# Kernel optimization log

Measured on AMD Instinct MI355X. Metric: run time of the kernel, lower is better.

The kernel has to match this reference:

```python
import jax, jax.numpy as jnp
import numpy as np


def _diffuse(x, A):
    # x: [B,C,N,L], A: [B,V,W] -> out[b,c,v,l] = sum_w x[b,c,w,l] * A[b,v,w]
    return jnp.einsum('ncwl,nvw->ncvl', x, A)


def setup_inputs() -> dict:
    key = jax.random.key(0)
    kx, k0, k1, k2, kw = jax.random.split(key, 5)
    B, C, N, L = 32, 40, 512, 12
    C_OUT = 20
    C_CAT = 7 * C  # (order*support_len + 1) * c_in = (2*3+1)*40
    x = jax.random.normal(kx, (B, C, N, L), dtype=jnp.float32)
    def mk_support(k):
        a = jax.random.uniform(k, (B, N, N), dtype=jnp.float32)
        return a / jnp.sum(a, axis=-1, keepdims=True)  # row-normalized transition
    A0, A1, A2 = mk_support(k0), mk_support(k1), mk_support(k2)
    # Conv2d(c_cat, c_out, kernel=(1,2), dilation=2) weights, stored [c_out, c_cat, 2]
    W = jax.random.normal(kw, (C_OUT, C_CAT, 2), dtype=jnp.float32) * 0.05
    b = jnp.zeros((C_OUT,), dtype=jnp.float32)
    return {'x': x, 'A0': A0, 'A1': A1, 'A2': A2, 'W': W, 'b': b}


def reference(x, A0, A1, A2, W, b):
    # dgcn.forward (eval mode, dropout is identity): order=2, support_len=3
    out = [x]
    for A in (A0, A1, A2):
        x1 = _diffuse(x, A)
        out.append(x1)
        x2 = _diffuse(x1, A)
        out.append(x2)
    h = jnp.concatenate(out, axis=1)  # [B, 7C, N, L]
    # linear_: Conv2d kernel (1,2), dilation 2, no padding -> taps at t and t+2, L_out = L-2
    y = (jnp.einsum('ncvl,oc->novl', h[..., :-2], W[:, :, 0])
         + jnp.einsum('ncvl,oc->novl', h[..., 2:], W[:, :, 1])
         + b[None, :, None, None])
    return y
```

## Files before the change

kernel.cpp:

```cpp
#include <hip/hip_runtime.h>
#include <hip/hip_bf16.h>


typedef unsigned short u16;
typedef u16 u16x4 __attribute__((ext_vector_type(4)));
typedef u16 u16x8 __attribute__((ext_vector_type(8)));
typedef __bf16 bf16x8 __attribute__((ext_vector_type(8)));
typedef float f32x4 __attribute__((ext_vector_type(4)));

__device__ __forceinline__ u16 f2bf(float f) {
    unsigned int u = __float_as_uint(f);
    u += 0x7fffu + ((u >> 16) & 1u);
    return (u16)(u >> 16);
}
__device__ __forceinline__ float bf2f(u16 h) {
    return __uint_as_float(((unsigned int)h) << 16);
}

__global__ __launch_bounds__(256) void proj_x(
    const float* __restrict__ x, const float* __restrict__ W,
    u16* __restrict__ P1, u16* __restrict__ P2, float* __restrict__ proj0)
{
    __shared__ u16 sA[144 * 104];
    __shared__ u16 sB[64 * 104];
    const int t = threadIdx.x;
    const int v0 = blockIdx.x * 64, l = blockIdx.y, b = blockIdx.z;

    for (int id = t; id < 144 * 13; id += 256) {
        int m = id / 13, kc = id % 13, k0 = kc * 8;
        u16x8 val = {};
        if (m < 140 && k0 < 80) {
            int o = m % 20, sg = m / 20;
            const float* wp = W + o * 560 + sg * 80 + k0;
            float4 w0 = *(const float4*)wp;
            float4 w1 = *(const float4*)(wp + 4);
            val[0] = f2bf(w0.x); val[1] = f2bf(w0.y); val[2] = f2bf(w0.z); val[3] = f2bf(w0.w);
            val[4] = f2bf(w1.x); val[5] = f2bf(w1.y); val[6] = f2bf(w1.z); val[7] = f2bf(w1.w);
        }
        *(u16x8*)(&sA[m * 104 + k0]) = val;
    }
    for (int id = t; id < 5120; id += 256) {
        int v = id & 63, k = id >> 6;
        int c = k >> 1, tap = k & 1;
        float xv = x[((size_t)(b * 40 + c) * 512 + v0 + v) * 12 + l + 2 * tap];
        sB[v * 104 + k] = f2bf(xv);
    }
    for (int id = t; id < 64 * 3; id += 256) {
        int v = id / 3, j = id % 3;
        u16x8 z = {};
        *(u16x8*)(&sB[v * 104 + 80 + j * 8]) = z;
    }
    __syncthreads();

    const int lane = t & 63, wid = t >> 6;
    const int lrow = lane & 15, lk = (lane >> 4) * 8;
    f32x4 acc[9] = {};
    #pragma unroll
    for (int ks = 0; ks < 3; ++ks) {
        bf16x8 xf = *(const bf16x8*)(&sB[(wid * 16 + lrow) * 104 + ks * 32 + lk]);
        #pragma unroll
        for (int mf = 0; mf < 9; ++mf) {
            bf16x8 af = *(const bf16x8*)(&sA[(mf * 16 + lrow) * 104 + ks * 32 + lk]);
            acc[mf] = __builtin_amdgcn_mfma_f32_16x16x32_bf16(af, xf, acc[mf], 0, 0, 0);
        }
    }

    const int v = v0 + wid * 16 + lrow;
    const int r4 = (lane >> 4) * 4;
    #pragma unroll
    for (int mf = 0; mf < 9; ++mf)
        #pragma unroll
        for (int i = 0; i < 4; ++i) {
            int m = mf * 16 + r4 + i;
            if (m < 140) {
                int o = m % 20, sg = m / 20;
                float val = acc[mf][i];
                if (sg == 0) {
                    proj0[((size_t)(b * 20 + o) * 10 + l) * 512 + v] = val;
                } else {
                    int s = (sg - 1) >> 1;
                    u16* dst = ((sg - 1) & 1) ? P2 : P1;
                    dst[((size_t)(s * 32 + b) * 200 + o * 10 + l) * 512 + v] = f2bf(val);
                }
            }
        }
}

template <int EPI>
__device__ __forceinline__ void gemm_body(
    const float* __restrict__ A0, const float* __restrict__ A1, const float* __restrict__ A2,
    const u16* __restrict__ Xsrc, u16* __restrict__ Tdst, float* __restrict__ Ydst)
{
    __shared__ u16 sA[64 * 40];
    __shared__ u16 sX[112 * 40];

    const int bid = blockIdx.x + 8 * (blockIdx.y + 2 * blockIdx.z);
    const int eid = (bid & 7) * 192 + (bid >> 3);
    const int vblk = (eid & 7) * 64;
    const int colbase = ((eid >> 3) & 1) * 112;
    const int z = eid >> 4, s = z >> 5, b = z & 31;

    const float* Af = (s == 0 ? A0 : (s == 1 ? A1 : A2)) + (size_t)b * 512 * 512;
    const u16* Xb = Xsrc + (size_t)z * 200 * 512;

    const int t = threadIdx.x;
    const int lane = t & 63, wid = t >> 6;
    const int lrow = lane & 15, lk = (lane >> 4) * 8;

    const int arow = t >> 2, ap2 = t & 3;
    const int xrow0 = t >> 2, xp = t & 3;

    float4 ar0, ar1;
    u16x8 xr0, xr1;
    auto load_regs = [&](int kt) {
        const int w0 = kt * 32;
        const float* ap = Af + (size_t)(vblk + arow) * 512 + w0 + ap2 * 8;
        ar0 = *(const float4*)ap;
        ar1 = *(const float4*)(ap + 4);
        {
            int cg = colbase + xrow0;
            u16x8 zv = {};
            xr0 = (cg < 200) ? *(const u16x8*)(Xb + (size_t)cg * 512 + w0 + xp * 8) : zv;
        }
        if (t < 192) {
            int row = (t + 256) >> 2, p = (t + 256) & 3;
            int cg = colbase + row;
            u16x8 zv = {};
            xr1 = (cg < 200) ? *(const u16x8*)(Xb + (size_t)cg * 512 + w0 + p * 8) : zv;
        }
    };
    auto store_lds = [&]() {
        u16x8 pk = { f2bf(ar0.x), f2bf(ar0.y), f2bf(ar0.z), f2bf(ar0.w),
                     f2bf(ar1.x), f2bf(ar1.y), f2bf(ar1.z), f2bf(ar1.w) };
        *(u16x8*)(&sA[arow * 40 + ap2 * 8]) = pk;
        *(u16x8*)(&sX[xrow0 * 40 + xp * 8]) = xr0;
        if (t < 192) {
            int row = (t + 256) >> 2, p = (t + 256) & 3;
            *(u16x8*)(&sX[row * 40 + p * 8]) = xr1;
        }
    };

    f32x4 acc[7] = {};
    load_regs(0);
    for (int kt = 0; kt < 16; ++kt) {
        store_lds();
        __syncthreads();
        if (kt < 15) load_regs(kt + 1);
        bf16x8 af = *(const bf16x8*)(&sA[(wid * 16 + lrow) * 40 + lk]);
        #pragma unroll
        for (int cf = 0; cf < 7; ++cf) {
            bf16x8 xf = *(const bf16x8*)(&sX[(cf * 16 + lrow) * 40 + lk]);
            acc[cf] = __builtin_amdgcn_mfma_f32_16x16x32_bf16(xf, af, acc[cf], 0, 0, 0);
        }
        __syncthreads();
    }

    const int v = vblk + wid * 16 + (lane & 15);
    const int r4 = (lane >> 4) * 4;
    if (EPI == 0) {
        u16* Tz = Tdst + (size_t)z * 200 * 512;
        #pragma unroll
        for (int cf = 0; cf < 7; ++cf)
            #pragma unroll
            for (int i = 0; i < 4; ++i) {
                int col = colbase + cf * 16 + r4 + i;
                if (col < 200) {
                    size_t idx = (size_t)col * 512 + v;
                    Tz[idx] = f2bf(acc[cf][i] + bf2f(Tz[idx]));
                }
            }
    } else {
        float* Yz = Ydst + (size_t)z * 200 * 512;
        #pragma unroll
        for (int cf = 0; cf < 7; ++cf)
            #pragma unroll
            for (int i = 0; i < 4; ++i) {
                int col = colbase + cf * 16 + r4 + i;
                if (col < 200)
                    Yz[(size_t)col * 512 + v] = acc[cf][i];
            }
    }
}

__global__ __launch_bounds__(256) void gemm_t(
    const float* __restrict__ A0, const float* __restrict__ A1, const float* __restrict__ A2,
    const u16* __restrict__ P2, u16* __restrict__ T)
{
    gemm_body<0>(A0, A1, A2, P2, T, nullptr);
}

__global__ __launch_bounds__(256) void gemm_yp(
    const float* __restrict__ A0, const float* __restrict__ A1, const float* __restrict__ A2,
    const u16* __restrict__ T, float* __restrict__ Ypart)
{
    gemm_body<1>(A0, A1, A2, T, nullptr, Ypart);
}

__global__ __launch_bounds__(256) void reduce_y(
    const float* __restrict__ Ypart, const float* __restrict__ proj0,
    const float* __restrict__ bias, float* __restrict__ y)
{
    int i = blockIdx.x * 256 + threadIdx.x;
    if (i >= 32 * 20 * 512) return;
    int v = i & 511;
    int r = i >> 9;
    int o = r % 20, b = r / 20;
    float bb = bias[o];
    float* yp = y + ((size_t)r * 512 + v) * 10;
    #pragma unroll
    for (int l = 0; l < 10; ++l) {
        float sum = proj0[((size_t)r * 10 + l) * 512 + v] + bb;
        #pragma unroll
        for (int s = 0; s < 3; ++s)
            sum += Ypart[((size_t)(s * 32 + b) * 200 + o * 10 + l) * 512 + v];
        yp[l] = sum;
    }
}

extern "C" void kernel_launch(void* const* d_in, const int* in_sizes, int n_in,
                              void* d_out, int out_size, void* d_ws, size_t ws_size,
                              hipStream_t stream) {
    const float* x    = (const float*)d_in[0];
    const float* A0   = (const float*)d_in[1];
    const float* A1   = (const float*)d_in[2];
    const float* A2   = (const float*)d_in[3];
    const float* W    = (const float*)d_in[4];
    const float* bias = (const float*)d_in[5];
    float* y = (float*)d_out;

    const size_t PSZ = (size_t)96 * 200 * 512;
    u16* P1 = (u16*)d_ws;
    u16* P2 = P1 + PSZ;
    float* proj0 = (float*)(P2 + PSZ);
    float* Ypart = proj0 + (size_t)32 * 20 * 10 * 512;

    proj_x<<<dim3(8, 10, 32), 256, 0, stream>>>(x, W, P1, P2, proj0);
    gemm_t<<<dim3(8, 2, 96), 256, 0, stream>>>(A0, A1, A2, P2, P1);
    gemm_yp<<<dim3(8, 2, 96), 256, 0, stream>>>(A0, A1, A2, P1, Ypart);
    reduce_y<<<dim3(1280), 256, 0, stream>>>(Ypart, proj0, bias, y);
}
```

Before: 121.0 us.

## Double-buffer diffusion GEMM with direct global-to-LDS loads and larger row tiles

The two diffusion GEMM kernels now stage A (kept as fp32) and X tiles straight from global memory into LDS with global_load_lds, into double buffers. The next k-tile load overlaps the MFMA work on the current one, and only one barrier is needed per iteration. Each block now covers 128 rows of v instead of 64, with an XOR swizzle on the fp32 A tile. A is converted to bf16 when read from LDS rather than before the LDS store. The X loads drop the col<200 guard, so the padded rows read neighbouring workspace data, but those results are discarded. The cost is more LDS per block, which may lower occupancy.

Result: faster. 107.5 us (-11.1%).

```diff
diff --git a/kernel.cpp b/kernel.cpp
--- a/kernel.cpp
+++ b/kernel.cpp
@@ -7,6 +7,10 @@
 typedef u16 u16x8 __attribute__((ext_vector_type(8)));
 typedef __bf16 bf16x8 __attribute__((ext_vector_type(8)));
 typedef float f32x4 __attribute__((ext_vector_type(4)));
+
+#define GLD_LDS16(g, l)  __builtin_amdgcn_global_load_lds( \
+    (const __attribute__((address_space(1))) void*)(g),    \
+    (__attribute__((address_space(3))) void*)(l), 16, 0, 0)
 
 __device__ __forceinline__ u16 f2bf(float f) {
     unsigned int u = __float_as_uint(f);
@@ -91,94 +95,107 @@
     const float* __restrict__ A0, const float* __restrict__ A1, const float* __restrict__ A2,
     const u16* __restrict__ Xsrc, u16* __restrict__ Tdst, float* __restrict__ Ydst)
 {
-    __shared__ u16 sA[64 * 40];
-    __shared__ u16 sX[112 * 40];
-
-    const int bid = blockIdx.x + 8 * (blockIdx.y + 2 * blockIdx.z);
-    const int eid = (bid & 7) * 192 + (bid >> 3);
-    const int vblk = (eid & 7) * 64;
-    const int colbase = ((eid >> 3) & 1) * 112;
-    const int z = eid >> 4, s = z >> 5, b = z & 31;
+    __shared__ float sAf[2][128 * 32];
+    __shared__ u16   sXs[2][112 * 32];
+
+    const int bid = blockIdx.x;
+    const int eid = (bid & 7) * 96 + (bid >> 3);
+    const int z = eid >> 3, rem = eid & 7;
+    const int vblk = (rem >> 1) * 128;
+    const int colbase = (rem & 1) * 112;
+    const int s = z >> 5, b = z & 31;
 
     const float* Af = (s == 0 ? A0 : (s == 1 ? A1 : A2)) + (size_t)b * 512 * 512;
     const u16* Xb = Xsrc + (size_t)z * 200 * 512;
 
     const int t = threadIdx.x;
     const int lane = t & 63, wid = t >> 6;
-    const int lrow = lane & 15, lk = (lane >> 4) * 8;
-
-    const int arow = t >> 2, ap2 = t & 3;
-    const int xrow0 = t >> 2, xp = t & 3;
-
-    float4 ar0, ar1;
-    u16x8 xr0, xr1;
-    auto load_regs = [&](int kt) {
+    const int lr = lane & 15;
+    const int kc0 = (lane >> 4) * 2;
+
+    auto stage = [&](int kt, int buf) {
         const int w0 = kt * 32;
-        const float* ap = Af + (size_t)(vblk + arow) * 512 + w0 + ap2 * 8;
-        ar0 = *(const float4*)ap;
-        ar1 = *(const float4*)(ap + 4);
-        {
-            int cg = colbase + xrow0;
-            u16x8 zv = {};
-            xr0 = (cg < 200) ? *(const u16x8*)(Xb + (size_t)cg * 512 + w0 + xp * 8) : zv;
-        }
-        if (t < 192) {
-            int row = (t + 256) >> 2, p = (t + 256) & 3;
-            int cg = colbase + row;
-            u16x8 zv = {};
-            xr1 = (cg < 200) ? *(const u16x8*)(Xb + (size_t)cg * 512 + w0 + p * 8) : zv;
+        float* ab = &sAf[buf][0];
+        u16*   xb = &sXs[buf][0];
+        #pragma unroll
+        for (int i = 0; i < 4; ++i) {
+            int op  = wid * 4 + i;
+            int row = op * 8 + (lane >> 3);
+            int pc  = lane & 7;
+            const float* src = Af + (size_t)(vblk + row) * 512 + w0 + ((pc ^ (row & 7)) << 2);
+            GLD_LDS16(src, ab + op * 256);
+        }
+        #pragma unroll
+        for (int i = 0; i < 2; ++i) {
+            int op = wid + i * 4;
+            if (op < 7) {
+                int row = op * 16 + (lane >> 2);
+                int ch  = lane & 3;
+                const u16* src = Xb + (size_t)(colbase + row) * 512 + w0 + ch * 8;
+                GLD_LDS16(src, xb + op * 512);
+            }
         }
     };
-    auto store_lds = [&]() {
-        u16x8 pk = { f2bf(ar0.x), f2bf(ar0.y), f2bf(ar0.z), f2bf(ar0.w),
-                     f2bf(ar1.x), f2bf(ar1.y), f2bf(ar1.z), f2bf(ar1.w) };
-        *(u16x8*)(&sA[arow * 40 + ap2 * 8]) = pk;
-        *(u16x8*)(&sX[xrow0 * 40 + xp * 8]) = xr0;
-        if (t < 192) {
-            int row = (t + 256) >> 2, p = (t + 256) & 3;
-            *(u16x8*)(&sX[row * 40 + p * 8]) = xr1;
-        }
-    };
-
-    f32x4 acc[7] = {};
-    load_regs(0);
+
+    f32x4 acc[7][2] = {};
+
+    stage(0, 0);
+    __syncthreads();
+
     for (int kt = 0; kt < 16; ++kt) {
-        store_lds();
+        const int cur = kt & 1;
+        if (kt < 15) stage(kt + 1, cur ^ 1);
+
+        bf16x8 af[2];
+        #pragma unroll
+        for (int mf = 0; mf < 2; ++mf) {
+            int r = wid * 32 + mf * 16 + lr;
+            const float* rb = &sAf[cur][r * 32];
+            f32x4 a0 = *(const f32x4*)(rb + ((kc0 ^ (r & 7)) << 2));
+            f32x4 a1 = *(const f32x4*)(rb + (((kc0 + 1) ^ (r & 7)) << 2));
+            union { u16x8 u; bf16x8 bv; } cv;
+            cv.u = (u16x8){ f2bf(a0[0]), f2bf(a0[1]), f2bf(a0[2]), f2bf(a0[3]),
+                            f2bf(a1[0]), f2bf(a1[1]), f2bf(a1[2]), f2bf(a1[3]) };
+            af[mf] = cv.bv;
+        }
+        #pragma unroll
+        for (int cf = 0; cf < 7; ++cf) {
+            bf16x8 xf = *(const bf16x8*)(&sXs[cur][(cf * 16 + lr) * 32 + (lane >> 4) * 8]);
+            #pragma unroll
+            for (int mf = 0; mf < 2; ++mf)
+                acc[cf][mf] = __builtin_amdgcn_mfma_f32_16x16x32_bf16(
+                    xf, af[mf], acc[cf][mf], 0, 0, 0);
+        }
         __syncthreads();
-        if (kt < 15) load_regs(kt + 1);
-        bf16x8 af = *(const bf16x8*)(&sA[(wid * 16 + lrow) * 40 + lk]);
-        #pragma unroll
-        for (int cf = 0; cf < 7; ++cf) {
-            bf16x8 xf = *(const bf16x8*)(&sX[(cf * 16 + lrow) * 40 + lk]);
-            acc[cf] = __builtin_amdgcn_mfma_f32_16x16x32_bf16(xf, af, acc[cf], 0, 0, 0);
-        }
-        __syncthreads();
-    }
-
-    const int v = vblk + wid * 16 + (lane & 15);
+    }
+
     const int r4 = (lane >> 4) * 4;
     if (EPI == 0) {
         u16* Tz = Tdst + (size_t)z * 200 * 512;
         #pragma unroll
         for (int cf = 0; cf < 7; ++cf)
             #pragma unroll
-            for (int i = 0; i < 4; ++i) {
-                int col = colbase + cf * 16 + r4 + i;
-                if (col < 200) {
-                    size_t idx = (size_t)col * 512 + v;
-                    Tz[idx] = f2bf(acc[cf][i] + bf2f(Tz[idx]));
+            for (int mf = 0; mf < 2; ++mf)
+                #pragma unroll
+                for (int i = 0; i < 4; ++i) {
+                    int col = colbase + cf * 16 + r4 + i;
+                    if (col < 200) {
+                        size_t idx = (size_t)col * 512 + vblk + wid * 32 + mf * 16 + lr;
+                        Tz[idx] = f2bf(acc[cf][mf][i] + bf2f(Tz[idx]));
+                    }
                 }
-            }
     } else {
         float* Yz = Ydst + (size_t)z * 200 * 512;
         #pragma unroll
         for (int cf = 0; cf < 7; ++cf)
             #pragma unroll
-            for (int i = 0; i < 4; ++i) {
-                int col = colbase + cf * 16 + r4 + i;
-                if (col < 200)
-                    Yz[(size_t)col * 512 + v] = acc[cf][i];
-            }
+            for (int mf = 0; mf < 2; ++mf)
+                #pragma unroll
+                for (int i = 0; i < 4; ++i) {
+                    int col = colbase + cf * 16 + r4 + i;
+                    if (col < 200)
+                        Yz[(size_t)col * 512 + vblk + wid * 32 + mf * 16 + lr] = acc[cf][mf][i];
+                }
     }
 }
 
@@ -235,7 +252,7 @@
     float* Ypart = proj0 + (size_t)32 * 20 * 10 * 512;
 
     proj_x<<<dim3(8, 10, 32), 256, 0, stream>>>(x, W, P1, P2, proj0);
-    gemm_t<<<dim3(8, 2, 96), 256, 0, stream>>>(A0, A1, A2, P2, P1);
-    gemm_yp<<<dim3(8, 2, 96), 256, 0, stream>>>(A0, A1, A2, P1, Ypart);
+    gemm_t<<<dim3(768), 256, 0, stream>>>(A0, A1, A2, P2, P1);
+    gemm_yp<<<dim3(768), 256, 0, stream>>>(A0, A1, A2, P1, Ypart);
     reduce_y<<<dim3(1280), 256, 0, stream>>>(Ypart, proj0, bias, y);
 }
```
